# Kernel tuning notes

Measured on AMD Instinct MI355X. Metric: run time of the kernel, lower is better.

## Reference

```python
import jax, jax.numpy as jnp
import numpy as np

N = 100000      # nodes
E = 1600000     # edges (avg degree 16)
D_IN = 128
D_H = 128
D_OUT = 64


def setup_inputs() -> dict:
    key = jax.random.key(0)
    k1, k2, k3, k4, k5 = jax.random.split(key, 5)
    x = jax.random.normal(k1, (N, D_IN), dtype=jnp.float32)
    edge_row = jax.random.randint(k2, (E,), 0, N, dtype=jnp.int32)
    # guarantee every destination row has at least one neighbor (no div-by-zero)
    edge_row = edge_row.at[:N].set(jnp.arange(N, dtype=jnp.int32))
    edge_col = jax.random.randint(k3, (E,), 0, N, dtype=jnp.int32)
    # xavier_uniform init as in the torch module
    lim1 = float(np.sqrt(6.0 / (D_IN + D_H)))
    W1 = jax.random.uniform(k4, (D_IN, D_H), jnp.float32, -lim1, lim1)
    lim2 = float(np.sqrt(6.0 / (D_H + D_OUT)))
    W2 = jax.random.uniform(k5, (D_H, D_OUT), jnp.float32, -lim2, lim2)
    return {"x": x, "W1": W1, "W2": W2, "edge_row": edge_row, "edge_col": edge_col}


def _mean_aggregate(h, edge_row, edge_col):
    # spmm(adjacency, h) with binary COO adjacency: out[i] = sum_{(i,j) in E} h[j]
    support = jax.ops.segment_sum(h[edge_col], edge_row, num_segments=N)  # [N, d]
    num_neigh = jax.ops.segment_sum(
        jnp.ones((edge_row.shape[0],), dtype=h.dtype), edge_row, num_segments=N
    )  # [N] = adjacency.sum(dim=1)
    return support / num_neigh[:, None]


def reference(x, W1, W2, edge_row, edge_col):
    # layer 1: GraphSAGEConv + relu
    h = jax.nn.relu(_mean_aggregate(x @ W1, edge_row, edge_col))
    # layer 2 (last): GraphSAGEConv, no activation -> logits
    logits = _mean_aggregate(h @ W2, edge_row, edge_col)
    return logits
```

## Files before the change

### kernel.cpp

```cpp
#include <hip/hip_runtime.h>
#include <hip/hip_fp16.h>


#define DIN 128
#define DH 128
#define DOUT 64

#define BSH 8
#define COLB 17
#define COLM ((1 << COLB) - 1)
#define LRM ((1 << BSH) - 1)
#define CHUNK 2048
#define CH_PT 8

typedef __attribute__((ext_vector_type(8))) short short8;
typedef __attribute__((ext_vector_type(8))) _Float16 half8;
typedef __attribute__((ext_vector_type(4))) float floatx4;

__device__ __forceinline__ unsigned bfpack(float a, float b) {
    unsigned ua = __float_as_uint(a);
    unsigned ub = __float_as_uint(b);
    ua += 0x7fffu + ((ua >> 16) & 1u);
    ub += 0x7fffu + ((ub >> 16) & 1u);
    return (ua >> 16) | (ub & 0xffff0000u);
}
__device__ __forceinline__ unsigned short bf1(float a) {
    unsigned u = __float_as_uint(a);
    u += 0x7fffu + ((u >> 16) & 1u);
    return (unsigned short)(u >> 16);
}

__device__ __forceinline__ void acch2(__half2* a, uint4 v) {
    a[0] = __hadd2(a[0], *(const __half2*)&v.x);
    a[1] = __hadd2(a[1], *(const __half2*)&v.y);
    a[2] = __hadd2(a[2], *(const __half2*)&v.z);
    a[3] = __hadd2(a[3], *(const __half2*)&v.w);
}
__device__ __forceinline__ __half2 h2shfl_xor(__half2 v, int m) {
    int u = __shfl_xor(*(int*)&v, m);
    return *(__half2*)&u;
}
__device__ __forceinline__ unsigned h2bits(__half2 v) {
    return *(unsigned*)&v;
}
__device__ __forceinline__ __half2 h2zero() {
    unsigned z = 0u;
    return *(__half2*)&z;
}

__global__ __launch_bounds__(256) void k_prep(const float* __restrict__ W1,
                                              const float* __restrict__ W2,
                                              unsigned short* __restrict__ Wt1,
                                              unsigned short* __restrict__ Wt2) {
    int idx = blockIdx.x * 256 + threadIdx.x;
    if (idx < 128 * 128) {
        int k = idx >> 7, nn = idx & 127;
        Wt1[nn * 128 + k] = bf1(W1[idx]);
    }
    int i2 = idx - 128 * 128;
    if (i2 >= 0 && i2 < 128 * 64) {
        int k = i2 >> 6, nn = i2 & 63;
        Wt2[nn * 128 + k] = __half_as_ushort(__float2half(W2[i2]));
    }
}


__global__ __launch_bounds__(256) void k_hist(const int* __restrict__ row,
                                              int* __restrict__ HT,
                                              int E, int nb, int nch) {
    __shared__ int h[512];
    int t = threadIdx.x, c = blockIdx.x;
    for (int i = t; i < nb; i += 256) h[i] = 0;
    __syncthreads();
    int base = c * CHUNK;
#pragma unroll
    for (int i = 0; i < CH_PT; ++i) {
        int e = base + i * 256 + t;
        if (e < E) atomicAdd(&h[row[e] >> BSH], 1);
    }
    __syncthreads();
    for (int i = t; i < nb; i += 256) HT[(size_t)i * nch + c] = h[i];
}

__global__ __launch_bounds__(256) void k_hscan_row(int* __restrict__ HT,
                                                   int* __restrict__ bsum,
                                                   int nch) {
    __shared__ int sh[256];
    int b = blockIdx.x, t = threadIdx.x;
    int carry = 0;
    for (int tile = 0; tile < nch; tile += 256) {
        int idx = tile + t;
        int v = (idx < nch) ? HT[(size_t)b * nch + idx] : 0;
        sh[t] = v;
        __syncthreads();
        for (int d = 1; d < 256; d <<= 1) {
            int u = (t >= d) ? sh[t - d] : 0;
            __syncthreads();
            sh[t] += u;
            __syncthreads();
        }
        if (idx < nch) HT[(size_t)b * nch + idx] = carry + sh[t] - v;
        carry += sh[255];
        __syncthreads();
    }
    if (t == 0) bsum[b] = carry;
}

__global__ __launch_bounds__(512) void k_hscan_base(const int* __restrict__ bsum,
                                                    int* __restrict__ bucketBase,
                                                    int nb, int E) {
    __shared__ int sh[512];
    int t = threadIdx.x;
    int v = (t < nb) ? bsum[t] : 0;
    sh[t] = v;
    __syncthreads();
    for (int d = 1; d < 512; d <<= 1) {
        int u = (t >= d) ? sh[t - d] : 0;
        __syncthreads();
        sh[t] += u;
        __syncthreads();
    }
    if (t < nb) bucketBase[t] = sh[t] - v;
    if (t == 0) bucketBase[nb] = E;
}

__global__ __launch_bounds__(256) void k_part(const int* __restrict__ row,
                                              const int* __restrict__ col,
                                              const int* __restrict__ HT,
                                              const int* __restrict__ bucketBase,
                                              int* __restrict__ packed,
                                              int E, int nb, int nch) {
    __shared__ int cur[512];
    int t = threadIdx.x, c = blockIdx.x;
    for (int i = t; i < nb; i += 256)
        cur[i] = HT[(size_t)i * nch + c] + bucketBase[i];
    __syncthreads();
    int base = c * CHUNK;
#pragma unroll
    for (int i = 0; i < CH_PT; ++i) {
        int e = base + i * 256 + t;
        if (e < E) {
            int r = row[e], cc = col[e];
            int b = r >> BSH;
            int pos = atomicAdd(&cur[b], 1);
            packed[pos] = ((r & LRM) << COLB) | cc;
        }
    }
}

__global__ __launch_bounds__(256) void k_build(const int* __restrict__ packed,
                                               const int* __restrict__ bucketBase,
                                               int* __restrict__ csr,
                                               int* __restrict__ offs,
                                               int* __restrict__ degc,
                                               float* __restrict__ invdeg,
                                               int N, int nb) {
    __shared__ int hist[256], scn[256], part[256];
    int t = threadIdx.x, b = blockIdx.x;
    int lo = bucketBase[b], hi = bucketBase[b + 1];
    int base_row = b << BSH;
    int nloc = N - base_row; if (nloc > 256) nloc = 256;
    hist[t] = 0;
    __syncthreads();
    for (int e = lo + t; e < hi; e += 256)
        atomicAdd(&hist[packed[e] >> COLB], 1);
    __syncthreads();
    int a = hist[t];
    part[t] = a;
    __syncthreads();
    for (int d = 1; d < 256; d <<= 1) {
        int v = (t >= d) ? part[t - d] : 0;
        __syncthreads();
        part[t] += v;
        __syncthreads();
    }
    scn[t] = part[t] - a;
    __syncthreads();
    for (int i = t; i < nloc; i += 256) {
        int r = base_row + i;
        offs[r] = lo + scn[i];
        int d = hist[i];
        degc[r] = d;
        invdeg[r] = 1.0f / (float)d;
    }
    __syncthreads();
    for (int e = lo + t; e < hi; e += 256) {
        int p = packed[e];
        int pos = lo + atomicAdd(&scn[p >> COLB], 1);
        csr[pos] = p & COLM;
    }
}


__global__ __launch_bounds__(256) void k_gemm1(const float* __restrict__ X,
                                               const unsigned short* __restrict__ Wt,
                                               unsigned short* __restrict__ H1h, int n) {
    __shared__ unsigned short xs[64][136];
    __shared__ unsigned short wt[128][136];
    int tid = threadIdx.x;
    int r0 = blockIdx.x * 64;

    for (int i = tid; i < 64 * 32; i += 256) {
        int r = i >> 5, c4 = i & 31;
        float4 v = make_float4(0.f, 0.f, 0.f, 0.f);
        if (r0 + r < n) v = ((const float4*)X)[(size_t)(r0 + r) * 32 + c4];
        *(uint2*)&xs[r][c4 * 4] = make_uint2(bfpack(v.x, v.y), bfpack(v.z, v.w));
    }
    for (int i = tid; i < 128 * 16; i += 256) {
        int r = i >> 4, c = i & 15;
        *(uint4*)&wt[r][c * 8] = ((const uint4*)Wt)[r * 16 + c];
    }
    __syncthreads();

    int w = tid >> 6, lane = tid & 63;
    int ml = lane & 15, q = lane >> 4;
    floatx4 acc[8];
#pragma unroll
    for (int t = 0; t < 8; ++t) acc[t] = (floatx4)(0.f);

#pragma unroll
    for (int kc = 0; kc < 4; ++kc) {
        short8 af = *(const short8*)&xs[w * 16 + ml][kc * 32 + q * 8];
#pragma unroll
        for (int nt = 0; nt < 8; ++nt) {
            short8 bf = *(const short8*)&wt[nt * 16 + ml][kc * 32 + q * 8];
            acc[nt] = __builtin_amdgcn_mfma_f32_16x16x32_bf16(af, bf, acc[nt], 0, 0, 0);
        }
    }
#pragma unroll
    for (int nt = 0; nt < 8; ++nt)
#pragma unroll
        for (int r = 0; r < 4; ++r) {
            int rr = r0 + w * 16 + q * 4 + r;
            if (rr < n)
                H1h[(size_t)rr * 128 + nt * 16 + ml] =
                    __half_as_ushort(__float2half(acc[nt][r]));
        }
}

__global__ __launch_bounds__(256) void k_gemm2(const unsigned* __restrict__ Hin,
                                               const unsigned short* __restrict__ Wt,
                                               unsigned short* __restrict__ H2h, int n) {
    __shared__ unsigned short xs[64][136];
    __shared__ unsigned short wt[64][136];
    int tid = threadIdx.x;
    int r0 = blockIdx.x * 64;

    for (int i = tid; i < 64 * 16; i += 256) {
        int r = i >> 4, c = i & 15;
        uint4 v = make_uint4(0u, 0u, 0u, 0u);
        if (r0 + r < n) v = ((const uint4*)Hin)[(size_t)(r0 + r) * 16 + c];
        *(uint4*)&xs[r][c * 8] = v;
    }
    for (int i = tid; i < 64 * 16; i += 256) {
        int r = i >> 4, c = i & 15;
        *(uint4*)&wt[r][c * 8] = ((const uint4*)Wt)[r * 16 + c];
    }
    __syncthreads();

    int w = tid >> 6, lane = tid & 63;
    int ml = lane & 15, q = lane >> 4;
    floatx4 acc[4];
#pragma unroll
    for (int t = 0; t < 4; ++t) acc[t] = (floatx4)(0.f);

#pragma unroll
    for (int kc = 0; kc < 4; ++kc) {
        half8 af = *(const half8*)&xs[w * 16 + ml][kc * 32 + q * 8];
#pragma unroll
        for (int nt = 0; nt < 4; ++nt) {
            half8 bf = *(const half8*)&wt[nt * 16 + ml][kc * 32 + q * 8];
            acc[nt] = __builtin_amdgcn_mfma_f32_16x16x32_f16(af, bf, acc[nt], 0, 0, 0);
        }
    }
#pragma unroll
    for (int nt = 0; nt < 4; ++nt)
#pragma unroll
        for (int r = 0; r < 4; ++r) {
            int rr = r0 + w * 16 + q * 4 + r;
            if (rr < n)
                H2h[(size_t)rr * 64 + nt * 16 + ml] =
                    __half_as_ushort(__float2half(acc[nt][r]));
        }
}


#define A1_SLOT(vv, s)                                                      \
    {                                                                       \
        int j = (s) * 4 + g;                                                \
        int c = __shfl(idx, (j < nd) ? j : 0);                              \
        vv = make_uint4(0u, 0u, 0u, 0u);                                    \
        if (j < nd) vv = H1h[((unsigned)c << 4) + sl];                      \
    }

__global__ __launch_bounds__(256) void k_agg1(const uint4* __restrict__ H1h,
                                              const int* __restrict__ offs,
                                              const int* __restrict__ degc,
                                              const float* __restrict__ invdeg,
                                              const int* __restrict__ csr,
                                              uint4* __restrict__ Hout, int n) {
    int wave = threadIdx.x >> 6, lane = threadIdx.x & 63;
    int row = blockIdx.x * 4 + wave;
    if (row >= n) return;
    int start = offs[row], d = degc[row];
    float inv = invdeg[row];
    int g = lane >> 4;
    int sl = lane & 15;

    int nd = d < 64 ? d : 64;
    int idx = (lane < nd) ? csr[start + lane] : 0;

    __half2 acc[4];
#pragma unroll
    for (int k = 0; k < 4; ++k) acc[k] = h2zero();

    uint4 v0, v1, v2, v3;
    A1_SLOT(v0, 0) A1_SLOT(v1, 1) A1_SLOT(v2, 2) A1_SLOT(v3, 3)
    acch2(acc, v0); acch2(acc, v1); acch2(acc, v2); acch2(acc, v3);
    if (nd > 16) {
        A1_SLOT(v0, 4) A1_SLOT(v1, 5) A1_SLOT(v2, 6) A1_SLOT(v3, 7)
        acch2(acc, v0); acch2(acc, v1); acch2(acc, v2); acch2(acc, v3);
    }
    if (nd > 32) {
        A1_SLOT(v0, 8) A1_SLOT(v1, 9) A1_SLOT(v2, 10) A1_SLOT(v3, 11)
        acch2(acc, v0); acch2(acc, v1); acch2(acc, v2); acch2(acc, v3);
    }
    if (nd > 48) {
        A1_SLOT(v0, 12) A1_SLOT(v1, 13) A1_SLOT(v2, 14) A1_SLOT(v3, 15)
        acch2(acc, v0); acch2(acc, v1); acch2(acc, v2); acch2(acc, v3);
    }
    if (d > 64) {
        for (int i = 64; i < d; i += 4) {
            int j = i + g;
            uint4 v = make_uint4(0u, 0u, 0u, 0u);
            if (j < d) {
                int c = csr[start + j];
                v = H1h[((unsigned)c << 4) + sl];
            }
            acch2(acc, v);
        }
    }

#pragma unroll
    for (int k = 0; k < 4; ++k) {
        acc[k] = __hadd2(acc[k], h2shfl_xor(acc[k], 16));
        acc[k] = __hadd2(acc[k], h2shfl_xor(acc[k], 32));
    }

    if (g == 0) {
        float f[8];
#pragma unroll
        for (int k = 0; k < 4; ++k) {
            f[2 * k]     = fmaxf(__low2float(acc[k]) * inv, 0.f);
            f[2 * k + 1] = fmaxf(__high2float(acc[k]) * inv, 0.f);
        }
        uint4 o;
        __half2 t0 = __floats2half2_rn(f[0], f[1]);
        __half2 t1 = __floats2half2_rn(f[2], f[3]);
        __half2 t2 = __floats2half2_rn(f[4], f[5]);
        __half2 t3 = __floats2half2_rn(f[6], f[7]);
        o.x = h2bits(t0); o.y = h2bits(t1); o.z = h2bits(t2); o.w = h2bits(t3);
        Hout[(size_t)row * 16 + sl] = o;
    }
}

#define A2_SLOT(vv, s)                                                      \
    {                                                                       \
        int j = (s) * 8 + g;                                                \
        int c = __shfl(idx, (j < nd) ? j : 0);                              \
        vv = make_uint4(0u, 0u, 0u, 0u);                                    \
        if (j < nd) vv = H2h[((unsigned)c << 3) + sl];                      \
    }

__global__ __launch_bounds__(256) void k_agg2(const uint4* __restrict__ H2h,
                                              const int* __restrict__ offs,
                                              const int* __restrict__ degc,
                                              const float* __restrict__ invdeg,
                                              const int* __restrict__ csr,
                                              float* __restrict__ Out, int n) {
    int wave = threadIdx.x >> 6, lane = threadIdx.x & 63;
    int row = blockIdx.x * 4 + wave;
    if (row >= n) return;
    int start = offs[row], d = degc[row];
    float inv = invdeg[row];
    int g = lane >> 3;
    int sl = lane & 7;

    int nd = d < 64 ? d : 64;
    int idx = (lane < nd) ? csr[start + lane] : 0;

    __half2 acc[4];
#pragma unroll
    for (int k = 0; k < 4; ++k) acc[k] = h2zero();

    uint4 v0, v1;
    A2_SLOT(v0, 0) A2_SLOT(v1, 1)
    acch2(acc, v0); acch2(acc, v1);
    if (nd > 16) {
        A2_SLOT(v0, 2) A2_SLOT(v1, 3)
        acch2(acc, v0); acch2(acc, v1);
    }
    if (nd > 32) {
        A2_SLOT(v0, 4) A2_SLOT(v1, 5)
        acch2(acc, v0); acch2(acc, v1);
    }
    if (nd > 48) {
        A2_SLOT(v0, 6) A2_SLOT(v1, 7)
        acch2(acc, v0); acch2(acc, v1);
    }
    if (d > 64) {
        for (int i = 64; i < d; i += 8) {
            int j = i + g;
            uint4 v = make_uint4(0u, 0u, 0u, 0u);
            if (j < d) {
                int c = csr[start + j];
                v = H2h[((unsigned)c << 3) + sl];
            }
            acch2(acc, v);
        }
    }

#pragma unroll
    for (int k = 0; k < 4; ++k) {
        acc[k] = __hadd2(acc[k], h2shfl_xor(acc[k], 8));
        acc[k] = __hadd2(acc[k], h2shfl_xor(acc[k], 16));
        acc[k] = __hadd2(acc[k], h2shfl_xor(acc[k], 32));
    }

    if (g == 0) {
        float4 o0, o1;
        o0.x = __low2float(acc[0]) * inv;  o0.y = __high2float(acc[0]) * inv;
        o0.z = __low2float(acc[1]) * inv;  o0.w = __high2float(acc[1]) * inv;
        o1.x = __low2float(acc[2]) * inv;  o1.y = __high2float(acc[2]) * inv;
        o1.z = __low2float(acc[3]) * inv;  o1.w = __high2float(acc[3]) * inv;
        ((float4*)Out)[(size_t)row * 16 + sl * 2]     = o0;
        ((float4*)Out)[(size_t)row * 16 + sl * 2 + 1] = o1;
    }
}

extern "C" void kernel_launch(void* const* d_in, const int* in_sizes, int n_in,
                              void* d_out, int out_size, void* d_ws, size_t ws_size,
                              hipStream_t stream) {
    const float* x    = (const float*)d_in[0];
    const float* W1   = (const float*)d_in[1];
    const float* W2   = (const float*)d_in[2];
    const int*   erow = (const int*)d_in[3];
    const int*   ecol = (const int*)d_in[4];
    const int N = in_sizes[0] / DIN;
    const int E = in_sizes[3];

    const int nb  = (N + (1 << BSH) - 1) >> BSH;
    const int nch = (E + CHUNK - 1) / CHUNK;

    size_t o = 0;
    auto take = [&](size_t nbytes) {
        void* p = (char*)d_ws + o;
        o += (nbytes + 255) & ~(size_t)255;
        return p;
    };
    int*            HT     = (int*)take((size_t)nb * nch * 4);
    int*            bsum   = (int*)take((size_t)nb * 4);
    int*            bbase  = (int*)take((size_t)(nb + 1) * 4);
    int*            packed = (int*)take((size_t)E * 4);
    int*            csr    = (int*)take((size_t)E * 4);
    int*            offs   = (int*)take((size_t)N * 4);
    int*            degc   = (int*)take((size_t)N * 4);
    float*          invdeg = (float*)take((size_t)N * 4);
    unsigned short* Wt1    = (unsigned short*)take(128 * 128 * 2);
    unsigned short* Wt2    = (unsigned short*)take(64 * 128 * 2);
    unsigned short* h1h    = (unsigned short*)take((size_t)N * DH * 2);
    unsigned*       h      = (unsigned*)take((size_t)N * DH * 2);
    unsigned short* h2h    = h1h;

    k_prep      <<<96,  256, 0, stream>>>(W1, W2, Wt1, Wt2);
    k_hist      <<<nch, 256, 0, stream>>>(erow, HT, E, nb, nch);
    k_hscan_row <<<nb,  256, 0, stream>>>(HT, bsum, nch);
    k_hscan_base<<<1,   512, 0, stream>>>(bsum, bbase, nb, E);
    k_part      <<<nch, 256, 0, stream>>>(erow, ecol, HT, bbase, packed, E, nb, nch);
    k_build     <<<nb,  256, 0, stream>>>(packed, bbase, csr, offs, degc, invdeg, N, nb);
    k_gemm1<<<(N + 63) / 64, 256, 0, stream>>>(x, Wt1, h1h, N);
    k_agg1 <<<(N + 3) / 4, 256, 0, stream>>>((const uint4*)h1h, offs, degc, invdeg,
                                             csr, (uint4*)h, N);
    k_gemm2<<<(N + 63) / 64, 256, 0, stream>>>(h, Wt2, h2h, N);
    k_agg2 <<<(N + 3) / 4, 256, 0, stream>>>((const uint4*)h2h, offs, degc,
                                             invdeg, csr, (float*)d_out, N);
}
```

Measured before the change: 267.0 us.

## Replace bucketed two-pass CSR build with global-atomic degree count and scatter

Drops the bucket histogram, partition and per-bucket local sort pipeline that built the CSR. It now counts degrees with global atomics, runs a three-level prefix scan over nodes, and fills the CSR by scattering with global atomic cursors. This cuts the number of passes and the packed intermediate buffer. In exchange it relies on contended global atomics and random scatter writes. Neighbor order within a row also becomes nondeterministic, which can change how the fp sums round.

```diff
diff --git a/kernel.cpp b/kernel.cpp
--- a/kernel.cpp
+++ b/kernel.cpp
@@ -5,13 +5,6 @@
 #define DIN 128
 #define DH 128
 #define DOUT 64
-
-#define BSH 8
-#define COLB 17
-#define COLM ((1 << COLB) - 1)
-#define LRM ((1 << BSH) - 1)
-#define CHUNK 2048
-#define CH_PT 8
 
 typedef __attribute__((ext_vector_type(8))) short short8;
 typedef __attribute__((ext_vector_type(8))) _Float16 half8;
@@ -51,8 +44,10 @@
 __global__ __launch_bounds__(256) void k_prep(const float* __restrict__ W1,
                                               const float* __restrict__ W2,
                                               unsigned short* __restrict__ Wt1,
-                                              unsigned short* __restrict__ Wt2) {
+                                              unsigned short* __restrict__ Wt2,
+                                              int* __restrict__ degc, int N) {
     int idx = blockIdx.x * 256 + threadIdx.x;
+    if (idx < N) degc[idx] = 0;
     if (idx < 128 * 128) {
         int k = idx >> 7, nn = idx & 127;
         Wt1[nn * 128 + k] = bf1(W1[idx]);
@@ -65,129 +60,68 @@
 }
 
 
-__global__ __launch_bounds__(256) void k_hist(const int* __restrict__ row,
-                                              int* __restrict__ HT,
-                                              int E, int nb, int nch) {
-    __shared__ int h[512];
-    int t = threadIdx.x, c = blockIdx.x;
-    for (int i = t; i < nb; i += 256) h[i] = 0;
-    __syncthreads();
-    int base = c * CHUNK;
-#pragma unroll
-    for (int i = 0; i < CH_PT; ++i) {
-        int e = base + i * 256 + t;
-        if (e < E) atomicAdd(&h[row[e] >> BSH], 1);
-    }
-    __syncthreads();
-    for (int i = t; i < nb; i += 256) HT[(size_t)i * nch + c] = h[i];
-}
-
-__global__ __launch_bounds__(256) void k_hscan_row(int* __restrict__ HT,
-                                                   int* __restrict__ bsum,
-                                                   int nch) {
-    __shared__ int sh[256];
-    int b = blockIdx.x, t = threadIdx.x;
-    int carry = 0;
-    for (int tile = 0; tile < nch; tile += 256) {
-        int idx = tile + t;
-        int v = (idx < nch) ? HT[(size_t)b * nch + idx] : 0;
-        sh[t] = v;
-        __syncthreads();
-        for (int d = 1; d < 256; d <<= 1) {
-            int u = (t >= d) ? sh[t - d] : 0;
-            __syncthreads();
-            sh[t] += u;
-            __syncthreads();
-        }
-        if (idx < nch) HT[(size_t)b * nch + idx] = carry + sh[t] - v;
-        carry += sh[255];
-        __syncthreads();
-    }
-    if (t == 0) bsum[b] = carry;
-}
-
-__global__ __launch_bounds__(512) void k_hscan_base(const int* __restrict__ bsum,
-                                                    int* __restrict__ bucketBase,
-                                                    int nb, int E) {
-    __shared__ int sh[512];
+__global__ __launch_bounds__(256) void k_deg(const int* __restrict__ row,
+                                             int* __restrict__ degc, int E) {
+    int e = blockIdx.x * 256 + threadIdx.x;
+    if (e < E) atomicAdd(&degc[row[e]], 1);
+}
+
+__global__ __launch_bounds__(1024) void k_scan1(const int* __restrict__ degc,
+                                                int* __restrict__ offs,
+                                                int* __restrict__ bsum, int N) {
+    __shared__ int sh[1024];
     int t = threadIdx.x;
-    int v = (t < nb) ? bsum[t] : 0;
+    int base = blockIdx.x * 1024;
+    int v = (base + t < N) ? degc[base + t] : 0;
     sh[t] = v;
     __syncthreads();
-    for (int d = 1; d < 512; d <<= 1) {
+    for (int d = 1; d < 1024; d <<= 1) {
         int u = (t >= d) ? sh[t - d] : 0;
         __syncthreads();
         sh[t] += u;
         __syncthreads();
     }
-    if (t < nb) bucketBase[t] = sh[t] - v;
-    if (t == 0) bucketBase[nb] = E;
-}
-
-__global__ __launch_bounds__(256) void k_part(const int* __restrict__ row,
+    if (base + t < N) offs[base + t] = sh[t] - v;
+    if (t == 1023) bsum[blockIdx.x] = sh[1023];
+}
+
+__global__ __launch_bounds__(128) void k_scan2(int* __restrict__ bsum, int nsb) {
+    __shared__ int sh[128];
+    int t = threadIdx.x;
+    int v = (t < nsb) ? bsum[t] : 0;
+    sh[t] = v;
+    __syncthreads();
+    for (int d = 1; d < 128; d <<= 1) {
+        int u = (t >= d) ? sh[t - d] : 0;
+        __syncthreads();
+        sh[t] += u;
+        __syncthreads();
+    }
+    if (t < nsb) bsum[t] = sh[t] - v;
+}
+
+__global__ __launch_bounds__(256) void k_scan3(int* __restrict__ offs,
+                                               const int* __restrict__ bsum,
+                                               const int* __restrict__ degc,
+                                               int* __restrict__ cur,
+                                               float* __restrict__ invdeg, int N) {
+    int i = blockIdx.x * 256 + threadIdx.x;
+    if (i < N) {
+        int o = offs[i] + bsum[i >> 10];
+        offs[i] = o;
+        cur[i] = o;
+        invdeg[i] = 1.0f / (float)degc[i];
+    }
+}
+
+__global__ __launch_bounds__(256) void k_fill(const int* __restrict__ row,
                                               const int* __restrict__ col,
-                                              const int* __restrict__ HT,
-                                              const int* __restrict__ bucketBase,
-                                              int* __restrict__ packed,
-                                              int E, int nb, int nch) {
-    __shared__ int cur[512];
-    int t = threadIdx.x, c = blockIdx.x;
-    for (int i = t; i < nb; i += 256)
-        cur[i] = HT[(size_t)i * nch + c] + bucketBase[i];
-    __syncthreads();
-    int base = c * CHUNK;
-#pragma unroll
-    for (int i = 0; i < CH_PT; ++i) {
-        int e = base + i * 256 + t;
-        if (e < E) {
-            int r = row[e], cc = col[e];
-            int b = r >> BSH;
-            int pos = atomicAdd(&cur[b], 1);
-            packed[pos] = ((r & LRM) << COLB) | cc;
-        }
-    }
-}
-
-__global__ __launch_bounds__(256) void k_build(const int* __restrict__ packed,
-                                               const int* __restrict__ bucketBase,
-                                               int* __restrict__ csr,
-                                               int* __restrict__ offs,
-                                               int* __restrict__ degc,
-                                               float* __restrict__ invdeg,
-                                               int N, int nb) {
-    __shared__ int hist[256], scn[256], part[256];
-    int t = threadIdx.x, b = blockIdx.x;
-    int lo = bucketBase[b], hi = bucketBase[b + 1];
-    int base_row = b << BSH;
-    int nloc = N - base_row; if (nloc > 256) nloc = 256;
-    hist[t] = 0;
-    __syncthreads();
-    for (int e = lo + t; e < hi; e += 256)
-        atomicAdd(&hist[packed[e] >> COLB], 1);
-    __syncthreads();
-    int a = hist[t];
-    part[t] = a;
-    __syncthreads();
-    for (int d = 1; d < 256; d <<= 1) {
-        int v = (t >= d) ? part[t - d] : 0;
-        __syncthreads();
-        part[t] += v;
-        __syncthreads();
-    }
-    scn[t] = part[t] - a;
-    __syncthreads();
-    for (int i = t; i < nloc; i += 256) {
-        int r = base_row + i;
-        offs[r] = lo + scn[i];
-        int d = hist[i];
-        degc[r] = d;
-        invdeg[r] = 1.0f / (float)d;
-    }
-    __syncthreads();
-    for (int e = lo + t; e < hi; e += 256) {
-        int p = packed[e];
-        int pos = lo + atomicAdd(&scn[p >> COLB], 1);
-        csr[pos] = p & COLM;
+                                              int* __restrict__ cur,
+                                              int* __restrict__ csr, int E) {
+    int e = blockIdx.x * 256 + threadIdx.x;
+    if (e < E) {
+        int pos = atomicAdd(&cur[row[e]], 1);
+        csr[pos] = col[e];
     }
 }
 
@@ -449,8 +383,7 @@
     const int N = in_sizes[0] / DIN;
     const int E = in_sizes[3];
 
-    const int nb  = (N + (1 << BSH) - 1) >> BSH;
-    const int nch = (E + CHUNK - 1) / CHUNK;
+    const int nsb = (N + 1023) >> 10;
 
     size_t o = 0;
     auto take = [&](size_t nbytes) {
@@ -458,13 +391,11 @@
         o += (nbytes + 255) & ~(size_t)255;
         return p;
     };
-    int*            HT     = (int*)take((size_t)nb * nch * 4);
-    int*            bsum   = (int*)take((size_t)nb * 4);
-    int*            bbase  = (int*)take((size_t)(nb + 1) * 4);
-    int*            packed = (int*)take((size_t)E * 4);
     int*            csr    = (int*)take((size_t)E * 4);
     int*            offs   = (int*)take((size_t)N * 4);
     int*            degc   = (int*)take((size_t)N * 4);
+    int*            cur    = (int*)take((size_t)N * 4);
+    int*            bsum   = (int*)take((size_t)(nsb + 1) * 4);
     float*          invdeg = (float*)take((size_t)N * 4);
     unsigned short* Wt1    = (unsigned short*)take(128 * 128 * 2);
     unsigned short* Wt2    = (unsigned short*)take(64 * 128 * 2);
@@ -472,12 +403,12 @@
     unsigned*       h      = (unsigned*)take((size_t)N * DH * 2);
     unsigned short* h2h    = h1h;
 
-    k_prep      <<<96,  256, 0, stream>>>(W1, W2, Wt1, Wt2);
-    k_hist      <<<nch, 256, 0, stream>>>(erow, HT, E, nb, nch);
-    k_hscan_row <<<nb,  256, 0, stream>>>(HT, bsum, nch);
-    k_hscan_base<<<1,   512, 0, stream>>>(bsum, bbase, nb, E);
-    k_part      <<<nch, 256, 0, stream>>>(erow, ecol, HT, bbase, packed, E, nb, nch);
-    k_build     <<<nb,  256, 0, stream>>>(packed, bbase, csr, offs, degc, invdeg, N, nb);
+    k_prep <<<(N + 255) / 256, 256, 0, stream>>>(W1, W2, Wt1, Wt2, degc, N);
+    k_deg  <<<(E + 255) / 256, 256, 0, stream>>>(erow, degc, E);
+    k_scan1<<<nsb, 1024, 0, stream>>>(degc, offs, bsum, N);
+    k_scan2<<<1, 128, 0, stream>>>(bsum, nsb);
+    k_scan3<<<(N + 255) / 256, 256, 0, stream>>>(offs, bsum, degc, cur, invdeg, N);
+    k_fill <<<(E + 255) / 256, 256, 0, stream>>>(erow, ecol, cur, csr, E);
     k_gemm1<<<(N + 63) / 64, 256, 0, stream>>>(x, Wt1, h1h, N);
     k_agg1 <<<(N + 3) / 4, 256, 0, stream>>>((const uint4*)h1h, offs, degc, invdeg,
                                              csr, (uint4*)h, N);
```

New measurement: 401.9 us. 1.51x slower.
